# Kernel tuning notes

Hardware: AMD Instinct MI355X
Metric: run time of the kernel (lower is better)

Reference implementation:

```python
import jax, jax.numpy as jnp
import numpy as np
import math

B, S, DIM = 2, 2048, 2048
N_HEADS, N_KV_HEADS = 32, 8
HEAD_DIM = DIM // N_HEADS  # 64
N_REP = N_HEADS // N_KV_HEADS  # 4
NEG_INF = -1e9


def setup_inputs() -> dict:
    key = jax.random.key(0)
    ks = jax.random.split(key, 6)
    x = jax.random.normal(ks[0], (B, S, DIM), dtype=jnp.float32)
    # RoPE frequencies (standard Llama formulation)
    inv_freq = 1.0 / (10000.0 ** (np.arange(0, HEAD_DIM, 2, dtype=np.float32) / HEAD_DIM))
    t = np.arange(S, dtype=np.float32)
    freqs = np.outer(t, inv_freq)  # [S, HEAD_DIM//2]
    freqs_cos = jnp.asarray(np.cos(freqs), dtype=jnp.float32)
    freqs_sin = jnp.asarray(np.sin(freqs), dtype=jnp.float32)
    # additive causal mask [S, S]
    mask = jnp.where(jnp.tril(jnp.ones((S, S), dtype=bool)), 0.0, NEG_INF).astype(jnp.float32)
    sc = 1.0 / math.sqrt(DIM)
    wq = jax.random.normal(ks[1], (DIM, N_HEADS * HEAD_DIM), dtype=jnp.float32) * sc
    wk = jax.random.normal(ks[2], (DIM, N_KV_HEADS * HEAD_DIM), dtype=jnp.float32) * sc
    wv = jax.random.normal(ks[3], (DIM, N_KV_HEADS * HEAD_DIM), dtype=jnp.float32) * sc
    wo = jax.random.normal(ks[4], (N_HEADS * HEAD_DIM, DIM), dtype=jnp.float32) * sc
    return {"x": x, "freqs_cos": freqs_cos, "freqs_sin": freqs_sin, "mask": mask,
            "wq": wq, "wk": wk, "wv": wv, "wo": wo}


def _apply_rotary(x, cos, sin):
    # x: [B, S, H, HEAD_DIM]; cos/sin: [S, HEAD_DIM//2]
    b, s, h, d = x.shape
    xr = x.astype(jnp.float32).reshape(b, s, h, d // 2, 2)
    xe, xo = xr[..., 0], xr[..., 1]
    c = cos[None, :, None, :]
    sn = sin[None, :, None, :]
    oe = xe * c - xo * sn
    oo = xe * sn + xo * c
    out = jnp.stack([oe, oo], axis=-1).reshape(b, s, h, d)
    return out.astype(x.dtype)


def reference(x, freqs_cos, freqs_sin, mask, wq, wk, wv, wo):
    b, s, _ = x.shape
    xq = (x @ wq).reshape(b, s, N_HEADS, HEAD_DIM)
    xk = (x @ wk).reshape(b, s, N_KV_HEADS, HEAD_DIM)
    xv = (x @ wv).reshape(b, s, N_KV_HEADS, HEAD_DIM)
    xq = _apply_rotary(xq, freqs_cos, freqs_sin)
    xk = _apply_rotary(xk, freqs_cos, freqs_sin)
    # repeat_kv: [B, S, KVH, D] -> [B, S, H, D]
    keys = jnp.repeat(xk, N_REP, axis=2)
    values = jnp.repeat(xv, N_REP, axis=2)
    # [B, H, Q, K] scores (naive, materialized as in source)
    scores = jnp.einsum('bqhd,bkhd->bhqk', xq, keys) / math.sqrt(HEAD_DIM)
    scores = scores + mask[None, None, :, :]
    probs = jax.nn.softmax(scores.astype(jnp.float32), axis=-1).astype(xq.dtype)
    out = jnp.einsum('bhqk,bkhd->bqhd', probs, values).reshape(b, s, N_HEADS * HEAD_DIM)
    return out @ wo
```

## Files before the change

kernel.cpp:

```cpp
#include <hip/hip_runtime.h>
#include <hip/hip_bf16.h>

typedef __bf16 bf16x8 __attribute__((ext_vector_type(8)));
typedef float f32x4 __attribute__((ext_vector_type(4)));
typedef float f32x16 __attribute__((ext_vector_type(16)));
typedef short s16x4 __attribute__((ext_vector_type(4)));
typedef short s16x8 __attribute__((ext_vector_type(8)));

__device__ __forceinline__ short f2bf(float f) {
  union { __bf16 h; short s; } p; p.h = (__bf16)f; return p.s;
}
__device__ __forceinline__ float bf2f(short s) {
  union { unsigned u; float f; } v; v.u = ((unsigned)(unsigned short)s) << 16;
  return v.f;
}
__device__ __forceinline__ void gload16(const void* g, void* l) {
  __builtin_amdgcn_global_load_lds(
      (const __attribute__((address_space(1))) unsigned*)g,
      (__attribute__((address_space(3))) unsigned*)l, 16, 0, 0);
}
__device__ __forceinline__ unsigned pack2(float lo, float hi) {
  union { __bf16 h[2]; unsigned u; } p;
  p.h[0] = (__bf16)lo; p.h[1] = (__bf16)hi;
  return p.u;
}
__device__ __forceinline__ float vsum16(const f32x16& v) {
  const float a0 = v[0] + v[1], a1 = v[2] + v[3], a2 = v[4] + v[5], a3 = v[6] + v[7];
  const float a4 = v[8] + v[9], a5 = v[10] + v[11], a6 = v[12] + v[13], a7 = v[14] + v[15];
  return ((a0 + a1) + (a2 + a3)) + ((a4 + a5) + (a6 + a7));
}

constexpr float KSC = 0.18033688f;

__global__ __launch_bounds__(256) void prep_kernel(const float* __restrict__ x,
                                                   const float* __restrict__ wq,
                                                   const float* __restrict__ wk,
                                                   const float* __restrict__ wv,
                                                   const float* __restrict__ wo,
                                                   short* __restrict__ xb,
                                                   short* __restrict__ wqT,
                                                   short* __restrict__ wkT,
                                                   short* __restrict__ wvT,
                                                   short* __restrict__ woT) {
  __shared__ float T[32][33];
  const int z = blockIdx.z;
  if (z == 4) {
    const int bid = blockIdx.y * 64 + blockIdx.x;
    const int i0 = bid * 512 + threadIdx.x;
    #pragma unroll
    for (int q = 0; q < 2; ++q) {
      const int i = i0 + q * 256;
      const float4 v = reinterpret_cast<const float4*>(x)[i];
      s16x4 o;
      o[0] = f2bf(v.x); o[1] = f2bf(v.y); o[2] = f2bf(v.z); o[3] = f2bf(v.w);
      reinterpret_cast<s16x4*>(xb)[i] = o;
    }
    return;
  }
  const float* W; short* WT; int N;
  if (z == 0)      { W = wq; WT = wqT; N = 2048; }
  else if (z == 1) { W = wk; WT = wkT; N = 512; }
  else if (z == 2) { W = wv; WT = wvT; N = 512; }
  else             { W = wo; WT = woT; N = 2048; }
  const int k0 = blockIdx.x * 32, n0 = blockIdx.y * 32;
  if (n0 >= N) return;
  const int r = threadIdx.x >> 5, c = threadIdx.x & 31;
  #pragma unroll
  for (int q = 0; q < 4; ++q) T[r + q * 8][c] = W[(size_t)(k0 + r + q * 8) * N + n0 + c];
  __syncthreads();
  #pragma unroll
  for (int q = 0; q < 4; ++q)
    WT[(size_t)(n0 + r + q * 8) * 2048 + k0 + c] = f2bf(T[c][r + q * 8]);
}

__global__ void rope_k(short* __restrict__ K, const float* __restrict__ cosT,
                       const float* __restrict__ sinT) {
  const int i = blockIdx.x * blockDim.x + threadIdx.x;
  const int s = (i >> 6) & 2047;
  const int p0 = (i & 7) * 4;
  s16x8 v = *reinterpret_cast<const s16x8*>(&K[(size_t)i * 8]);
  #pragma unroll
  for (int jj = 0; jj < 4; ++jj) {
    const float c = cosT[s * 32 + p0 + jj];
    const float sn = sinT[s * 32 + p0 + jj];
    const float e = bf2f(v[2 * jj]), o = bf2f(v[2 * jj + 1]);
    v[2 * jj] = f2bf(e * c - o * sn);
    v[2 * jj + 1] = f2bf(e * sn + o * c);
  }
  *reinterpret_cast<s16x8*>(&K[(size_t)i * 8]) = v;
}

template <int BM, int EPI>
__global__ __launch_bounds__(512, 2) void gemm256(const short* __restrict__ A,
                                                  const short* __restrict__ BT,
                                                  void* __restrict__ C0,
                                                  void* __restrict__ C1,
                                                  void* __restrict__ C2,
                                                  int M, int N, int K) {
  constexpr int BN = 256, BK = 64;
  constexpr int AIT = (BM * 8) / 512;
  constexpr int MREP = BM / 32;
  __shared__ short As[2][BM * BK];
  __shared__ short Bs[2][BN * BK];
  const int tid = threadIdx.x, lane = tid & 63, wid = tid >> 6;
  const int wm = wid >> 2, wn = wid & 3;
  const int lr = lane & 15, hi2 = lane >> 4;

  const int nwg = gridDim.x * gridDim.y;
  int bid = blockIdx.y * gridDim.x + blockIdx.x;
  bid = (bid & 7) * (nwg >> 3) + (bid >> 3);
  const int row0 = (bid % gridDim.x) * BM;
  const int col0 = (bid / gridDim.x) * BN;

  size_t aSrc[AIT]; int aDst[AIT];
  size_t bSrc[4];   int bDst[4];
  #pragma unroll
  for (int i = 0; i < AIT; ++i) {
    const int c = i * 512 + tid, r = c >> 3, ch = c & 7;
    aSrc[i] = (size_t)(row0 + r) * K + (ch ^ (r & 7)) * 8;
    aDst[i] = c * 8;
  }
  #pragma unroll
  for (int i = 0; i < 4; ++i) {
    const int c = i * 512 + tid, r = c >> 3, ch = c & 7;
    bSrc[i] = (size_t)(col0 + r) * K + (ch ^ (r & 7)) * 8;
    bDst[i] = c * 8;
  }

  f32x4 acc[MREP][4] = {};

  const int NT = K / BK;
  #pragma unroll
  for (int i = 0; i < AIT; ++i) gload16(&A[aSrc[i]], &As[0][aDst[i]]);
  #pragma unroll
  for (int i = 0; i < 4; ++i) gload16(&BT[bSrc[i]], &Bs[0][bDst[i]]);

  int buf = 0;
  for (int t = 0; t < NT; ++t) {
    __syncthreads();
    if (t + 1 < NT) {
      const int k1 = (t + 1) * BK;
      #pragma unroll
      for (int i = 0; i < AIT; ++i) gload16(&A[aSrc[i] + k1], &As[buf ^ 1][aDst[i]]);
      #pragma unroll
      for (int i = 0; i < 4; ++i) gload16(&BT[bSrc[i] + k1], &Bs[buf ^ 1][bDst[i]]);
    }
    #pragma unroll
    for (int ks = 0; ks < 2; ++ks) {
      const int sw = ((ks * 4 + hi2) ^ (lr & 7)) * 8;
      bf16x8 af[MREP], bfr[4];
      #pragma unroll
      for (int m = 0; m < MREP; ++m)
        af[m] = *reinterpret_cast<const bf16x8*>(
            &As[buf][(wm * (BM / 2) + m * 16 + lr) * BK + sw]);
      #pragma unroll
      for (int n = 0; n < 4; ++n)
        bfr[n] = *reinterpret_cast<const bf16x8*>(
            &Bs[buf][(wn * 64 + n * 16 + lr) * BK + sw]);
      __builtin_amdgcn_s_setprio(1);
      #pragma unroll
      for (int m = 0; m < MREP; ++m)
        #pragma unroll
        for (int n = 0; n < 4; ++n)
          acc[m][n] = __builtin_amdgcn_mfma_f32_16x16x32_bf16(af[m], bfr[n], acc[m][n], 0, 0, 0);
      __builtin_amdgcn_s_setprio(0);
    }
    buf ^= 1;
  }

  const int lc = lane & 15, lr4 = (lane >> 4) * 4;
  if constexpr (EPI == 1) {
    #pragma unroll
    for (int m = 0; m < MREP; ++m)
      #pragma unroll
      for (int n = 0; n < 4; ++n)
        #pragma unroll
        for (int i = 0; i < 4; ++i) {
          const int row = row0 + wm * (BM / 2) + m * 16 + lr4 + i;
          const int col = col0 + wn * 64 + n * 16 + lc;
          ((float*)C0)[(size_t)row * N + col] = acc[m][n][i];
        }
  } else {
    #pragma unroll
    for (int m = 0; m < MREP; ++m) {
      #pragma unroll
      for (int n = 0; n < 4; ++n) {
        const int row = row0 + wm * (BM / 2) + m * 16 + lr4;
        const int col = col0 + wn * 64 + n * 16 + lc;
        if (col0 < 2048) {
          #pragma unroll
          for (int i = 0; i < 4; ++i)
            ((short*)C0)[(size_t)(row + i) * 2048 + col] = f2bf(acc[m][n][i]);
        } else if (col0 < 2560) {
          #pragma unroll
          for (int i = 0; i < 4; ++i)
            ((short*)C1)[(size_t)(row + i) * 512 + (col - 2048)] = f2bf(acc[m][n][i]);
        } else {
          const int c2 = col - 2560;
          const int kvh = c2 >> 6, d = c2 & 63;
          const int bb = row >> 11, st = row & 2047;
          s16x4 o4;
          #pragma unroll
          for (int i = 0; i < 4; ++i) o4[i] = f2bf(acc[m][n][i]);
          *reinterpret_cast<s16x4*>(
              &((short*)C2)[((size_t)(bb * 8 + kvh) * 64 + d) * 2048 + st]) = o4;
        }
      }
    }
  }
}


__device__ __forceinline__ void rope_qfrag(bf16x8 qf[4], const float* __restrict__ cosT,
                                           const float* __restrict__ sinT, int qrow, int hi) {
  #pragma unroll
  for (int ds = 0; ds < 4; ++ds) {
    const int p0 = ds * 8 + hi * 4;
    const float4 cv = *reinterpret_cast<const float4*>(&cosT[qrow * 32 + p0]);
    const float4 sv = *reinterpret_cast<const float4*>(&sinT[qrow * 32 + p0]);
    const float ca[4] = {cv.x, cv.y, cv.z, cv.w};
    const float sa[4] = {sv.x, sv.y, sv.z, sv.w};
    union { bf16x8 v; s16x8 s; } u; u.v = qf[ds];
    s16x8 r;
    #pragma unroll
    for (int jj = 0; jj < 4; ++jj) {
      const float c = ca[jj] * KSC;
      const float sn = sa[jj] * KSC;
      const float e = bf2f(u.s[2 * jj]), o = bf2f(u.s[2 * jj + 1]);
      r[2 * jj] = f2bf(e * c - o * sn);
      r[2 * jj + 1] = f2bf(e * sn + o * c);
    }
    union { s16x8 s; bf16x8 v; } w; w.s = r;
    qf[ds] = w.v;
  }
}

template <bool MASKED>
__device__ __forceinline__ void ptile(const short* __restrict__ Ksb,
                                      const short* __restrict__ Vsb,
                                      const bf16x8 qf[4], int kb, int qrow,
                                      int l31, int hi,
                                      f32x16& o0, f32x16& o1, float& l_r) {
  f32x16 sa0 = {}, sa1 = {};
  __builtin_amdgcn_s_setprio(1);
  #pragma unroll
  for (int ds = 0; ds < 4; ++ds) {
    const int c0 = ((ds * 2 + hi) ^ (l31 & 7)) * 8;
    const bf16x8 kf0 = *reinterpret_cast<const bf16x8*>(&Ksb[l31 * 64 + c0]);
    const bf16x8 kf1 = *reinterpret_cast<const bf16x8*>(&Ksb[(32 + l31) * 64 + c0]);
    sa0 = __builtin_amdgcn_mfma_f32_32x32x16_bf16(kf0, qf[ds], sa0, 0, 0, 0);
    sa1 = __builtin_amdgcn_mfma_f32_32x32x16_bf16(kf1, qf[ds], sa1, 0, 0, 0);
  }
  __builtin_amdgcn_s_setprio(0);
  if (MASKED) {
    #pragma unroll
    for (int r = 0; r < 16; ++r) {
      const int kk = kb + (r & 3) + 8 * (r >> 2) + 4 * hi;
      if (kk > qrow) sa0[r] = -1e30f;
      if (kk + 32 > qrow) sa1[r] = -1e30f;
    }
  }
  #pragma unroll
  for (int r = 0; r < 16; ++r) {
    sa0[r] = exp2f(sa0[r]);
    sa1[r] = exp2f(sa1[r]);
  }
  l_r += vsum16(sa0) + vsum16(sa1);
  bf16x8 paf[4];
  #pragma unroll
  for (int ks = 0; ks < 4; ++ks) {
    union { unsigned w[4]; bf16x8 v; } u;
    #pragma unroll
    for (int w2 = 0; w2 < 4; ++w2) {
      const int rbase = (ks & 1) * 8 + w2 * 2;
      if (ks < 2) u.w[w2] = pack2(sa0[rbase], sa0[rbase + 1]);
      else        u.w[w2] = pack2(sa1[rbase], sa1[rbase + 1]);
    }
    paf[ks] = u.v;
  }
  __builtin_amdgcn_s_setprio(1);
  #pragma unroll
  for (int ks = 0; ks < 4; ++ks) {
    const int g0 = ((2 * ks) ^ (l31 & 7)) * 8 + hi * 4;
    const int g1 = ((2 * ks + 1) ^ (l31 & 7)) * 8 + hi * 4;
    union { s16x4 h2[2]; bf16x8 v; } a0, a1;
    a0.h2[0] = *reinterpret_cast<const s16x4*>(&Vsb[l31 * 64 + g0]);
    a0.h2[1] = *reinterpret_cast<const s16x4*>(&Vsb[l31 * 64 + g1]);
    a1.h2[0] = *reinterpret_cast<const s16x4*>(&Vsb[(32 + l31) * 64 + g0]);
    a1.h2[1] = *reinterpret_cast<const s16x4*>(&Vsb[(32 + l31) * 64 + g1]);
    o0 = __builtin_amdgcn_mfma_f32_32x32x16_bf16(a0.v, paf[ks], o0, 0, 0, 0);
    o1 = __builtin_amdgcn_mfma_f32_32x32x16_bf16(a1.v, paf[ks], o1, 0, 0, 0);
  }
  __builtin_amdgcn_s_setprio(0);
}

template <bool MA>
__device__ __forceinline__ void ptile2(const short* __restrict__ Ksb,
                                       const short* __restrict__ Vsb,
                                       const bf16x8 qfA[4], const bf16x8 qfB[4],
                                       int kb, int qrowA, int l31, int hi,
                                       f32x16& oA0, f32x16& oA1, f32x16& oB0, f32x16& oB1,
                                       float& lA, float& lB) {
  f32x16 a0 = {}, a1 = {}, b0 = {}, b1 = {};
  __builtin_amdgcn_s_setprio(1);
  #pragma unroll
  for (int ds = 0; ds < 4; ++ds) {
    const int c0 = ((ds * 2 + hi) ^ (l31 & 7)) * 8;
    const bf16x8 kf0 = *reinterpret_cast<const bf16x8*>(&Ksb[l31 * 64 + c0]);
    const bf16x8 kf1 = *reinterpret_cast<const bf16x8*>(&Ksb[(32 + l31) * 64 + c0]);
    a0 = __builtin_amdgcn_mfma_f32_32x32x16_bf16(kf0, qfA[ds], a0, 0, 0, 0);
    b0 = __builtin_amdgcn_mfma_f32_32x32x16_bf16(kf0, qfB[ds], b0, 0, 0, 0);
    a1 = __builtin_amdgcn_mfma_f32_32x32x16_bf16(kf1, qfA[ds], a1, 0, 0, 0);
    b1 = __builtin_amdgcn_mfma_f32_32x32x16_bf16(kf1, qfB[ds], b1, 0, 0, 0);
  }
  __builtin_amdgcn_s_setprio(0);
  if (MA) {
    #pragma unroll
    for (int r = 0; r < 16; ++r) {
      const int kk = kb + (r & 3) + 8 * (r >> 2) + 4 * hi;
      if (kk > qrowA) a0[r] = -1e30f;
      if (kk + 32 > qrowA) a1[r] = -1e30f;
    }
  }
  #pragma unroll
  for (int r = 0; r < 16; ++r) {
    a0[r] = exp2f(a0[r]);
    b0[r] = exp2f(b0[r]);
    a1[r] = exp2f(a1[r]);
    b1[r] = exp2f(b1[r]);
  }
  lA += vsum16(a0) + vsum16(a1);
  lB += vsum16(b0) + vsum16(b1);
  bf16x8 pafA[4], pafB[4];
  #pragma unroll
  for (int ks = 0; ks < 4; ++ks) {
    union { unsigned w[4]; bf16x8 v; } ua, ub;
    #pragma unroll
    for (int w2 = 0; w2 < 4; ++w2) {
      const int rbase = (ks & 1) * 8 + w2 * 2;
      if (ks < 2) { ua.w[w2] = pack2(a0[rbase], a0[rbase + 1]);
                    ub.w[w2] = pack2(b0[rbase], b0[rbase + 1]); }
      else        { ua.w[w2] = pack2(a1[rbase], a1[rbase + 1]);
                    ub.w[w2] = pack2(b1[rbase], b1[rbase + 1]); }
    }
    pafA[ks] = ua.v; pafB[ks] = ub.v;
  }
  __builtin_amdgcn_s_setprio(1);
  #pragma unroll
  for (int ks = 0; ks < 4; ++ks) {
    const int g0 = ((2 * ks) ^ (l31 & 7)) * 8 + hi * 4;
    const int g1 = ((2 * ks + 1) ^ (l31 & 7)) * 8 + hi * 4;
    union { s16x4 h2[2]; bf16x8 v; } v0, v1;
    v0.h2[0] = *reinterpret_cast<const s16x4*>(&Vsb[l31 * 64 + g0]);
    v0.h2[1] = *reinterpret_cast<const s16x4*>(&Vsb[l31 * 64 + g1]);
    v1.h2[0] = *reinterpret_cast<const s16x4*>(&Vsb[(32 + l31) * 64 + g0]);
    v1.h2[1] = *reinterpret_cast<const s16x4*>(&Vsb[(32 + l31) * 64 + g1]);
    oA0 = __builtin_amdgcn_mfma_f32_32x32x16_bf16(v0.v, pafA[ks], oA0, 0, 0, 0);
    oB0 = __builtin_amdgcn_mfma_f32_32x32x16_bf16(v0.v, pafB[ks], oB0, 0, 0, 0);
    oA1 = __builtin_amdgcn_mfma_f32_32x32x16_bf16(v1.v, pafA[ks], oA1, 0, 0, 0);
    oB1 = __builtin_amdgcn_mfma_f32_32x32x16_bf16(v1.v, pafB[ks], oB1, 0, 0, 0);
  }
  __builtin_amdgcn_s_setprio(0);
}

__global__ __launch_bounds__(256, 2) void attn4(const short* __restrict__ Q,
                                                const short* __restrict__ K,
                                                const short* __restrict__ VT,
                                                const float* __restrict__ cosT,
                                                const float* __restrict__ sinT,
                                                short* __restrict__ O) {
  constexpr int S = 2048, H = 32;
  const int pair = blockIdx.x, kvh = blockIdx.y;
  const int b = blockIdx.z >> 1, rowhalf = blockIdx.z & 1;
  const int tid = threadIdx.x, lane = tid & 63, wid = tid >> 6;
  const int h = kvh * 4 + wid;
  const int l31 = lane & 31, hi = lane >> 5;
  const int qpA = pair, qpB = 31 - pair;
  const int q0A = qpA * 64 + rowhalf * 32, q0B = qpB * 64 + rowhalf * 32;
  const int qrowA = q0A + l31, qrowB = q0B + l31;
  const int bk = b * 8 + kvh;

  __shared__ short Ks[2][8192];
  __shared__ short Vs[2][8192];

  bf16x8 qfA[4], qfB[4];
  {
    const size_t qa = ((size_t)(b * S + qrowA) * H + h) * 64;
    const size_t qb = ((size_t)(b * S + qrowB) * H + h) * 64;
    #pragma unroll
    for (int ds = 0; ds < 4; ++ds) {
      qfA[ds] = *reinterpret_cast<const bf16x8*>(&Q[qa + ds * 16 + hi * 8]);
      qfB[ds] = *reinterpret_cast<const bf16x8*>(&Q[qb + ds * 16 + hi * 8]);
    }
    rope_qfrag(qfA, cosT, sinT, qrowA, hi);
    rope_qfrag(qfB, cosT, sinT, qrowB, hi);
  }

  f32x16 oA0 = {}, oA1 = {}, oB0 = {}, oB1 = {};
  float lA = 0.f, lB = 0.f;

  const int njt = (qpB + 2) >> 1;
  const size_t kroot = ((size_t)b * S * 8 + kvh) * 64;
  const size_t vroot = (size_t)bk * 64 * S;

  auto stage = [&](int j, int bufi) {
    #pragma unroll
    for (int s = 0; s < 2; ++s) {
      #pragma unroll
      for (int i = 0; i < 2; ++i) {
        const int c = i * 256 + tid;
        const int r = c >> 3, ch = c & 7;
        const int cs8 = (ch ^ (r & 7)) * 8;
        gload16(&K[kroot + (size_t)(j * 128 + s * 64 + r) * 512 + cs8],
                &Ks[bufi][s * 4096 + c * 8]);
        gload16(&VT[vroot + (size_t)r * S + j * 128 + s * 64 + cs8],
                &Vs[bufi][s * 4096 + c * 8]);
      }
    }
  };

  stage(0, 0);
  __syncthreads();

  int cur = 0;
  for (int j = 0; j < njt; ++j) {
    if (j + 1 < njt) stage(j + 1, cur ^ 1);
    #pragma unroll
    for (int s = 0; s < 2; ++s) {
      const int kb = j * 128 + s * 64;
      const short* Ksb = &Ks[cur][s * 4096];
      const short* Vsb = &Vs[cur][s * 4096];
      if (kb <= q0A + 31) {
        if (kb + 63 <= q0A)
          ptile2<false>(Ksb, Vsb, qfA, qfB, kb, qrowA, l31, hi,
                        oA0, oA1, oB0, oB1, lA, lB);
        else
          ptile2<true>(Ksb, Vsb, qfA, qfB, kb, qrowA, l31, hi,
                       oA0, oA1, oB0, oB1, lA, lB);
      } else if (kb <= q0B + 31) {
        if (kb + 63 <= q0B)
          ptile<false>(Ksb, Vsb, qfB, kb, qrowB, l31, hi, oB0, oB1, lB);
        else
          ptile<true>(Ksb, Vsb, qfB, kb, qrowB, l31, hi, oB0, oB1, lB);
      }
    }
    __syncthreads();
    cur ^= 1;
  }

  lA += __shfl_xor(lA, 32, 64);
  lB += __shfl_xor(lB, 32, 64);
  {
    const float inv = 1.f / lA;
    const size_t obase = ((size_t)(b * S + qrowA) * H + h) * 64;
    #pragma unroll
    for (int g = 0; g < 4; ++g) {
      s16x4 s0v, s1v;
      #pragma unroll
      for (int i = 0; i < 4; ++i) {
        s0v[i] = f2bf(oA0[4 * g + i] * inv);
        s1v[i] = f2bf(oA1[4 * g + i] * inv);
      }
      *reinterpret_cast<s16x4*>(&O[obase + 8 * g + 4 * hi]) = s0v;
      *reinterpret_cast<s16x4*>(&O[obase + 32 + 8 * g + 4 * hi]) = s1v;
    }
  }
  {
    const float inv = 1.f / lB;
    const size_t obase = ((size_t)(b * S + qrowB) * H + h) * 64;
    #pragma unroll
    for (int g = 0; g < 4; ++g) {
      s16x4 s0v, s1v;
      #pragma unroll
      for (int i = 0; i < 4; ++i) {
        s0v[i] = f2bf(oB0[4 * g + i] * inv);
        s1v[i] = f2bf(oB1[4 * g + i] * inv);
      }
      *reinterpret_cast<s16x4*>(&O[obase + 8 * g + 4 * hi]) = s0v;
      *reinterpret_cast<s16x4*>(&O[obase + 32 + 8 * g + 4 * hi]) = s1v;
    }
  }
}

extern "C" void kernel_launch(void* const* d_in, const int* in_sizes, int n_in,
                              void* d_out, int out_size, void* d_ws, size_t ws_size,
                              hipStream_t stream) {
  const float* x  = (const float*)d_in[0];
  const float* fc = (const float*)d_in[1];
  const float* fs = (const float*)d_in[2];
  const float* wq = (const float*)d_in[4];
  const float* wk = (const float*)d_in[5];
  const float* wv = (const float*)d_in[6];
  const float* wo = (const float*)d_in[7];
  float* out = (float*)d_out;

  short* xb  = (short*)d_ws;
  short* wqT = xb  + 8388608;
  short* wkT = wqT + 4194304;
  short* wvT = wkT + 1048576;
  short* woT = wvT + 1048576;
  short* Qb  = woT + 4194304;
  short* Kb  = Qb  + 8388608;
  short* VTb = Kb  + 2097152;
  short* attb = xb;

  prep_kernel<<<dim3(64, 64, 5), 256, 0, stream>>>(x, wq, wk, wv, wo,
                                                   xb, wqT, wkT, wvT, woT);

  gemm256<256, 3><<<dim3(16, 12), 512, 0, stream>>>(xb, wqT, Qb, Kb, VTb, 4096, 3072, 2048);

  rope_k<<<1024, 256, 0, stream>>>(Kb, fc, fs);

  attn4<<<dim3(16, 8, 4), 256, 0, stream>>>(Qb, Kb, VTb, fc, fs, attb);

  gemm256<128, 1><<<dim3(32, 8), 512, 0, stream>>>(attb, woT, out, nullptr, nullptr, 4096, 2048, 2048);
}
```

Measured before the change: 226.6 us.

## Restructure causal attention into 512-thread blocks with per-wave query tiles

Replaces the attn4 kernel, where each wave processed two paired query tiles (A and B) with 128-key stages, with attn5. In attn5, 8 waves split into two groups that handle the mirrored 32-row query tiles p and 63-p, each sharing 64-key K/V stages in LDS. This halves per-wave accumulator registers and LDS per block, raising occupancy (launch bounds 512,4). In exchange, each K/V tile gets less reuse per LDS load, there are more sync barriers, and the two groups may be load-imbalanced within a block.

```diff
diff --git a/kernel.cpp b/kernel.cpp
--- a/kernel.cpp
+++ b/kernel.cpp
@@ -294,129 +294,48 @@
   __builtin_amdgcn_s_setprio(0);
 }
 
-template <bool MA>
-__device__ __forceinline__ void ptile2(const short* __restrict__ Ksb,
-                                       const short* __restrict__ Vsb,
-                                       const bf16x8 qfA[4], const bf16x8 qfB[4],
-                                       int kb, int qrowA, int l31, int hi,
-                                       f32x16& oA0, f32x16& oA1, f32x16& oB0, f32x16& oB1,
-                                       float& lA, float& lB) {
-  f32x16 a0 = {}, a1 = {}, b0 = {}, b1 = {};
-  __builtin_amdgcn_s_setprio(1);
-  #pragma unroll
-  for (int ds = 0; ds < 4; ++ds) {
-    const int c0 = ((ds * 2 + hi) ^ (l31 & 7)) * 8;
-    const bf16x8 kf0 = *reinterpret_cast<const bf16x8*>(&Ksb[l31 * 64 + c0]);
-    const bf16x8 kf1 = *reinterpret_cast<const bf16x8*>(&Ksb[(32 + l31) * 64 + c0]);
-    a0 = __builtin_amdgcn_mfma_f32_32x32x16_bf16(kf0, qfA[ds], a0, 0, 0, 0);
-    b0 = __builtin_amdgcn_mfma_f32_32x32x16_bf16(kf0, qfB[ds], b0, 0, 0, 0);
-    a1 = __builtin_amdgcn_mfma_f32_32x32x16_bf16(kf1, qfA[ds], a1, 0, 0, 0);
-    b1 = __builtin_amdgcn_mfma_f32_32x32x16_bf16(kf1, qfB[ds], b1, 0, 0, 0);
-  }
-  __builtin_amdgcn_s_setprio(0);
-  if (MA) {
-    #pragma unroll
-    for (int r = 0; r < 16; ++r) {
-      const int kk = kb + (r & 3) + 8 * (r >> 2) + 4 * hi;
-      if (kk > qrowA) a0[r] = -1e30f;
-      if (kk + 32 > qrowA) a1[r] = -1e30f;
-    }
-  }
-  #pragma unroll
-  for (int r = 0; r < 16; ++r) {
-    a0[r] = exp2f(a0[r]);
-    b0[r] = exp2f(b0[r]);
-    a1[r] = exp2f(a1[r]);
-    b1[r] = exp2f(b1[r]);
-  }
-  lA += vsum16(a0) + vsum16(a1);
-  lB += vsum16(b0) + vsum16(b1);
-  bf16x8 pafA[4], pafB[4];
-  #pragma unroll
-  for (int ks = 0; ks < 4; ++ks) {
-    union { unsigned w[4]; bf16x8 v; } ua, ub;
-    #pragma unroll
-    for (int w2 = 0; w2 < 4; ++w2) {
-      const int rbase = (ks & 1) * 8 + w2 * 2;
-      if (ks < 2) { ua.w[w2] = pack2(a0[rbase], a0[rbase + 1]);
-                    ub.w[w2] = pack2(b0[rbase], b0[rbase + 1]); }
-      else        { ua.w[w2] = pack2(a1[rbase], a1[rbase + 1]);
-                    ub.w[w2] = pack2(b1[rbase], b1[rbase + 1]); }
-    }
-    pafA[ks] = ua.v; pafB[ks] = ub.v;
-  }
-  __builtin_amdgcn_s_setprio(1);
-  #pragma unroll
-  for (int ks = 0; ks < 4; ++ks) {
-    const int g0 = ((2 * ks) ^ (l31 & 7)) * 8 + hi * 4;
-    const int g1 = ((2 * ks + 1) ^ (l31 & 7)) * 8 + hi * 4;
-    union { s16x4 h2[2]; bf16x8 v; } v0, v1;
-    v0.h2[0] = *reinterpret_cast<const s16x4*>(&Vsb[l31 * 64 + g0]);
-    v0.h2[1] = *reinterpret_cast<const s16x4*>(&Vsb[l31 * 64 + g1]);
-    v1.h2[0] = *reinterpret_cast<const s16x4*>(&Vsb[(32 + l31) * 64 + g0]);
-    v1.h2[1] = *reinterpret_cast<const s16x4*>(&Vsb[(32 + l31) * 64 + g1]);
-    oA0 = __builtin_amdgcn_mfma_f32_32x32x16_bf16(v0.v, pafA[ks], oA0, 0, 0, 0);
-    oB0 = __builtin_amdgcn_mfma_f32_32x32x16_bf16(v0.v, pafB[ks], oB0, 0, 0, 0);
-    oA1 = __builtin_amdgcn_mfma_f32_32x32x16_bf16(v1.v, pafA[ks], oA1, 0, 0, 0);
-    oB1 = __builtin_amdgcn_mfma_f32_32x32x16_bf16(v1.v, pafB[ks], oB1, 0, 0, 0);
-  }
-  __builtin_amdgcn_s_setprio(0);
-}
-
-__global__ __launch_bounds__(256, 2) void attn4(const short* __restrict__ Q,
+__global__ __launch_bounds__(512, 4) void attn5(const short* __restrict__ Q,
                                                 const short* __restrict__ K,
                                                 const short* __restrict__ VT,
                                                 const float* __restrict__ cosT,
                                                 const float* __restrict__ sinT,
                                                 short* __restrict__ O) {
   constexpr int S = 2048, H = 32;
-  const int pair = blockIdx.x, kvh = blockIdx.y;
-  const int b = blockIdx.z >> 1, rowhalf = blockIdx.z & 1;
+  const int p = blockIdx.x, kvh = blockIdx.y, b = blockIdx.z;
   const int tid = threadIdx.x, lane = tid & 63, wid = tid >> 6;
-  const int h = kvh * 4 + wid;
+  const int hg = wid & 3, ss = wid >> 2;
+  const int h = kvh * 4 + hg;
   const int l31 = lane & 31, hi = lane >> 5;
-  const int qpA = pair, qpB = 31 - pair;
-  const int q0A = qpA * 64 + rowhalf * 32, q0B = qpB * 64 + rowhalf * 32;
-  const int qrowA = q0A + l31, qrowB = q0B + l31;
+  const int qt = ss ? (63 - p) : p;
+  const int q0 = qt * 32;
+  const int qrow = q0 + l31;
   const int bk = b * 8 + kvh;
 
-  __shared__ short Ks[2][8192];
-  __shared__ short Vs[2][8192];
-
-  bf16x8 qfA[4], qfB[4];
+  __shared__ short Ks[2][4096];
+  __shared__ short Vs[2][4096];
+
+  bf16x8 qf[4];
   {
-    const size_t qa = ((size_t)(b * S + qrowA) * H + h) * 64;
-    const size_t qb = ((size_t)(b * S + qrowB) * H + h) * 64;
-    #pragma unroll
-    for (int ds = 0; ds < 4; ++ds) {
-      qfA[ds] = *reinterpret_cast<const bf16x8*>(&Q[qa + ds * 16 + hi * 8]);
-      qfB[ds] = *reinterpret_cast<const bf16x8*>(&Q[qb + ds * 16 + hi * 8]);
-    }
-    rope_qfrag(qfA, cosT, sinT, qrowA, hi);
-    rope_qfrag(qfB, cosT, sinT, qrowB, hi);
-  }
-
-  f32x16 oA0 = {}, oA1 = {}, oB0 = {}, oB1 = {};
-  float lA = 0.f, lB = 0.f;
-
-  const int njt = (qpB + 2) >> 1;
+    const size_t qa = ((size_t)(b * S + qrow) * H + h) * 64;
+    #pragma unroll
+    for (int ds = 0; ds < 4; ++ds)
+      qf[ds] = *reinterpret_cast<const bf16x8*>(&Q[qa + ds * 16 + hi * 8]);
+    rope_qfrag(qf, cosT, sinT, qrow, hi);
+  }
+
+  f32x16 o0 = {}, o1 = {};
+  float l_r = 0.f;
+
+  const int njt = ((2047 - 32 * p) >> 6) + 1;
   const size_t kroot = ((size_t)b * S * 8 + kvh) * 64;
   const size_t vroot = (size_t)bk * 64 * S;
 
+  const int sr = tid >> 3, sch = tid & 7;
+  const int cs8 = (sch ^ (sr & 7)) * 8;
+
   auto stage = [&](int j, int bufi) {
-    #pragma unroll
-    for (int s = 0; s < 2; ++s) {
-      #pragma unroll
-      for (int i = 0; i < 2; ++i) {
-        const int c = i * 256 + tid;
-        const int r = c >> 3, ch = c & 7;
-        const int cs8 = (ch ^ (r & 7)) * 8;
-        gload16(&K[kroot + (size_t)(j * 128 + s * 64 + r) * 512 + cs8],
-                &Ks[bufi][s * 4096 + c * 8]);
-        gload16(&VT[vroot + (size_t)r * S + j * 128 + s * 64 + cs8],
-                &Vs[bufi][s * 4096 + c * 8]);
-      }
-    }
+    gload16(&K[kroot + (size_t)(j * 64 + sr) * 512 + cs8], &Ks[bufi][tid * 8]);
+    gload16(&VT[vroot + (size_t)sr * S + j * 64 + cs8], &Vs[bufi][tid * 8]);
   };
 
   stage(0, 0);
@@ -425,60 +344,30 @@
   int cur = 0;
   for (int j = 0; j < njt; ++j) {
     if (j + 1 < njt) stage(j + 1, cur ^ 1);
-    #pragma unroll
-    for (int s = 0; s < 2; ++s) {
-      const int kb = j * 128 + s * 64;
-      const short* Ksb = &Ks[cur][s * 4096];
-      const short* Vsb = &Vs[cur][s * 4096];
-      if (kb <= q0A + 31) {
-        if (kb + 63 <= q0A)
-          ptile2<false>(Ksb, Vsb, qfA, qfB, kb, qrowA, l31, hi,
-                        oA0, oA1, oB0, oB1, lA, lB);
-        else
-          ptile2<true>(Ksb, Vsb, qfA, qfB, kb, qrowA, l31, hi,
-                       oA0, oA1, oB0, oB1, lA, lB);
-      } else if (kb <= q0B + 31) {
-        if (kb + 63 <= q0B)
-          ptile<false>(Ksb, Vsb, qfB, kb, qrowB, l31, hi, oB0, oB1, lB);
-        else
-          ptile<true>(Ksb, Vsb, qfB, kb, qrowB, l31, hi, oB0, oB1, lB);
-      }
+    const int kb = j * 64;
+    if (kb <= q0 + 31) {
+      if (kb + 63 <= q0)
+        ptile<false>(Ks[cur], Vs[cur], qf, kb, qrow, l31, hi, o0, o1, l_r);
+      else
+        ptile<true>(Ks[cur], Vs[cur], qf, kb, qrow, l31, hi, o0, o1, l_r);
     }
     __syncthreads();
     cur ^= 1;
   }
 
-  lA += __shfl_xor(lA, 32, 64);
-  lB += __shfl_xor(lB, 32, 64);
-  {
-    const float inv = 1.f / lA;
-    const size_t obase = ((size_t)(b * S + qrowA) * H + h) * 64;
-    #pragma unroll
-    for (int g = 0; g < 4; ++g) {
-      s16x4 s0v, s1v;
-      #pragma unroll
-      for (int i = 0; i < 4; ++i) {
-        s0v[i] = f2bf(oA0[4 * g + i] * inv);
-        s1v[i] = f2bf(oA1[4 * g + i] * inv);
-      }
-      *reinterpret_cast<s16x4*>(&O[obase + 8 * g + 4 * hi]) = s0v;
-      *reinterpret_cast<s16x4*>(&O[obase + 32 + 8 * g + 4 * hi]) = s1v;
-    }
-  }
-  {
-    const float inv = 1.f / lB;
-    const size_t obase = ((size_t)(b * S + qrowB) * H + h) * 64;
-    #pragma unroll
-    for (int g = 0; g < 4; ++g) {
-      s16x4 s0v, s1v;
-      #pragma unroll
-      for (int i = 0; i < 4; ++i) {
-        s0v[i] = f2bf(oB0[4 * g + i] * inv);
-        s1v[i] = f2bf(oB1[4 * g + i] * inv);
-      }
-      *reinterpret_cast<s16x4*>(&O[obase + 8 * g + 4 * hi]) = s0v;
-      *reinterpret_cast<s16x4*>(&O[obase + 32 + 8 * g + 4 * hi]) = s1v;
-    }
+  l_r += __shfl_xor(l_r, 32, 64);
+  const float inv = 1.f / l_r;
+  const size_t obase = ((size_t)(b * S + qrow) * H + h) * 64;
+  #pragma unroll
+  for (int g = 0; g < 4; ++g) {
+    s16x4 s0v, s1v;
+    #pragma unroll
+    for (int i = 0; i < 4; ++i) {
+      s0v[i] = f2bf(o0[4 * g + i] * inv);
+      s1v[i] = f2bf(o1[4 * g + i] * inv);
+    }
+    *reinterpret_cast<s16x4*>(&O[obase + 8 * g + 4 * hi]) = s0v;
+    *reinterpret_cast<s16x4*>(&O[obase + 32 + 8 * g + 4 * hi]) = s1v;
   }
 }
 
@@ -511,7 +400,7 @@
 
   rope_k<<<1024, 256, 0, stream>>>(Kb, fc, fs);
 
-  attn4<<<dim3(16, 8, 4), 256, 0, stream>>>(Qb, Kb, VTb, fc, fs, attb);
+  attn5<<<dim3(32, 8, 2), 512, 0, stream>>>(Qb, Kb, VTb, fc, fs, attb);
 
   gemm256<128, 1><<<dim3(32, 8), 512, 0, stream>>>(attb, woT, out, nullptr, nullptr, 4096, 2048, 2048);
 }
```

After: 225.8 us. About the same (-0.4%).
